# Kernel optimization log

Hardware: AMD Instinct MI355X
Metric: run time of the kernel (lower is better)

Reference implementation:

```python
import jax, jax.numpy as jnp
import numpy as np

EMBED_DIM = 1024
HIDDEN_DIM = 4096
NUM_EXPERTS = 8
TOP_K = 2


def setup_inputs() -> dict:
    key = jax.random.key(0)
    ks = jax.random.split(key, 5)
    x = jax.random.normal(ks[0], (2, 2048, EMBED_DIM), dtype=jnp.float32)
    Wg = jax.random.normal(ks[1], (EMBED_DIM, NUM_EXPERTS), dtype=jnp.float32) * 0.02
    W1 = jax.random.normal(ks[2], (NUM_EXPERTS, EMBED_DIM, HIDDEN_DIM), dtype=jnp.float32) * 0.02
    W3 = jax.random.normal(ks[3], (NUM_EXPERTS, EMBED_DIM, HIDDEN_DIM), dtype=jnp.float32) * 0.02
    W2 = jax.random.normal(ks[4], (NUM_EXPERTS, HIDDEN_DIM, EMBED_DIM), dtype=jnp.float32) * 0.02
    return {"x": x, "Wg": Wg, "W1": W1, "W3": W3, "W2": W2}


def reference(x, Wg, W1, W3, W2):
    # Gate: linear projection to num_experts logits
    gate = jnp.einsum("bsd,de->bse", x, Wg)  # [B,S,E]
    top_vals, top_idx = jax.lax.top_k(gate, TOP_K)  # [B,S,K]
    sel_w = jax.nn.softmax(top_vals, axis=-1)  # softmax over top-k values
    # Scatter selected weights into dense [B,S,E] (zeros for unselected experts)
    dense_w = jnp.sum(
        jax.nn.one_hot(top_idx, NUM_EXPERTS, dtype=sel_w.dtype) * sel_w[..., None],
        axis=-2,
    )  # [B,S,E]
    # Per-expert SwiGLU FFN; weight=0 for tokens not routed to expert e,
    # so the weighted-sum form is mathematically identical to masked dispatch.
    out = jnp.zeros_like(x)
    for e in range(NUM_EXPERTS):
        h = jax.nn.swish(jnp.einsum("bsd,dh->bsh", x, W1[e])) * jnp.einsum(
            "bsd,dh->bsh", x, W3[e]
        )
        out = out + dense_w[..., e:e + 1] * jnp.einsum("bsh,hd->bsd", h, W2[e])
    return out
```

## Files before the change

kernel.cpp:

```cpp
#include <hip/hip_runtime.h>
#include <hip/hip_bf16.h>
#include <stdint.h>

#define D_EMBED 1024
#define D_HID   4096
#define N_TOK   4096
#define N_EXP   8
#define CAP     4096
#define NROWA   8448

typedef __attribute__((ext_vector_type(4))) float f32x4;
typedef __attribute__((ext_vector_type(8))) short bf16x8;

__device__ __forceinline__ unsigned short f2bf(float f) {
    unsigned int u = __builtin_bit_cast(unsigned int, f);
    u += 0x7fffu + ((u >> 16) & 1u);
    return (unsigned short)(u >> 16);
}

__device__ __forceinline__ void gload_lds16(const void* g, void* l) {
    __builtin_amdgcn_global_load_lds(
        (const __attribute__((address_space(1))) unsigned int*)g,
        (__attribute__((address_space(3))) unsigned int*)l,
        16, 0, 0);
}

__global__ __launch_bounds__(256) void pack_w(const float* __restrict__ W,
                                              unsigned short* __restrict__ out, int R, int C) {
    int e = blockIdx.z, kb = blockIdx.y, cb = blockIdx.x;
    const float* Wp = W + (size_t)e * R * C + (size_t)(kb * 64) * C + cb * 64;
    unsigned short* op = out + (size_t)e * R * C;
    __shared__ unsigned short lds[64][72];
    int t = threadIdx.x;
    int r = t >> 2;
    int c0 = (t & 3) << 4;
    const float* src = Wp + (size_t)r * C + c0;
#pragma unroll
    for (int i = 0; i < 2; ++i) {
        f32x4 a = *reinterpret_cast<const f32x4*>(src + i * 8);
        f32x4 b = *reinterpret_cast<const f32x4*>(src + i * 8 + 4);
        bf16x8 o;
        o[0]=(short)f2bf(a[0]); o[1]=(short)f2bf(a[1]); o[2]=(short)f2bf(a[2]); o[3]=(short)f2bf(a[3]);
        o[4]=(short)f2bf(b[0]); o[5]=(short)f2bf(b[1]); o[6]=(short)f2bf(b[2]); o[7]=(short)f2bf(b[3]);
        *reinterpret_cast<bf16x8*>(&lds[r][c0 + i * 8]) = o;
    }
    __syncthreads();
#pragma unroll
    for (int i = 0; i < 2; ++i) {
        int cell = i * 256 + t;
        int ksl = cell >> 6, col = cell & 63;
        bf16x8 o;
#pragma unroll
        for (int j = 0; j < 8; ++j) o[j] = (short)lds[ksl * 8 + j][col];
        *reinterpret_cast<bf16x8*>(op + ((size_t)(kb * 8 + ksl) * C + cb * 64 + col) * 8) = o;
    }
}

__global__ __launch_bounds__(256) void pack_w13(const float* __restrict__ W1,
                                                const float* __restrict__ W3,
                                                unsigned short* __restrict__ out) {
    int e = blockIdx.z, kb = blockIdx.y, cb = blockIdx.x;
    size_t ebase = (size_t)e * D_EMBED * D_HID;
    const float* b1 = W1 + ebase + (size_t)(kb * 64) * D_HID + cb * 32;
    const float* b3 = W3 + ebase + (size_t)(kb * 64) * D_HID + cb * 32;
    unsigned short* op = out + (size_t)e * D_EMBED * 2 * D_HID;
    __shared__ unsigned short lds[64][72];
    int t = threadIdx.x;
    int r = t >> 2, ck = t & 3;
    const float* src = (ck >= 2 ? b3 : b1) + (size_t)r * D_HID + (ck & 1) * 16;
#pragma unroll
    for (int i = 0; i < 2; ++i) {
        f32x4 a = *reinterpret_cast<const f32x4*>(src + i * 8);
        f32x4 b = *reinterpret_cast<const f32x4*>(src + i * 8 + 4);
        bf16x8 o;
        o[0]=(short)f2bf(a[0]); o[1]=(short)f2bf(a[1]); o[2]=(short)f2bf(a[2]); o[3]=(short)f2bf(a[3]);
        o[4]=(short)f2bf(b[0]); o[5]=(short)f2bf(b[1]); o[6]=(short)f2bf(b[2]); o[7]=(short)f2bf(b[3]);
        *reinterpret_cast<bf16x8*>(&lds[r][ck * 16 + i * 8]) = o;
    }
    __syncthreads();
#pragma unroll
    for (int i = 0; i < 2; ++i) {
        int cell = i * 256 + t;
        int ksl = cell >> 6, pcp = cell & 63;
        int lcol = ((pcp >> 4) & 1) * 32 + ((pcp >> 5) & 1) * 16 + (pcp & 15);
        bf16x8 o;
#pragma unroll
        for (int j = 0; j < 8; ++j) o[j] = (short)lds[ksl * 8 + j][lcol];
        *reinterpret_cast<bf16x8*>(op + ((size_t)(kb * 8 + ksl) * (2 * D_HID) + cb * 64 + pcp) * 8) = o;
    }
}

__global__ __launch_bounds__(256) void gate_kernel(const float* __restrict__ x,
                                                   const float* __restrict__ Wg,
                                                   int* __restrict__ counts,
                                                   int* __restrict__ toks,
                                                   float* __restrict__ wgts,
                                                   int* __restrict__ slots) {
    int wave = threadIdx.x >> 6;
    int lane = threadIdx.x & 63;
    int tok = blockIdx.x * 4 + wave;
    const float* xp = x + (size_t)tok * D_EMBED;
    float acc[8] = {0, 0, 0, 0, 0, 0, 0, 0};
#pragma unroll
    for (int i = 0; i < 16; ++i) {
        int d = lane + 64 * i;
        float xv = xp[d];
        f32x4 w0 = *reinterpret_cast<const f32x4*>(Wg + (size_t)d * 8);
        f32x4 w1 = *reinterpret_cast<const f32x4*>(Wg + (size_t)d * 8 + 4);
        acc[0] += xv * w0[0]; acc[1] += xv * w0[1]; acc[2] += xv * w0[2]; acc[3] += xv * w0[3];
        acc[4] += xv * w1[0]; acc[5] += xv * w1[1]; acc[6] += xv * w1[2]; acc[7] += xv * w1[3];
    }
#pragma unroll
    for (int e = 0; e < 8; ++e)
        for (int s = 32; s; s >>= 1) acc[e] += __shfl_xor(acc[e], s, 64);
    if (lane == 0) {
        int i0 = 0; float v0 = acc[0];
#pragma unroll
        for (int e = 1; e < 8; ++e) if (acc[e] > v0) { v0 = acc[e]; i0 = e; }
        int i1 = -1; float v1 = -1e30f;
#pragma unroll
        for (int e = 0; e < 8; ++e) if (e != i0 && acc[e] > v1) { v1 = acc[e]; i1 = e; }
        float ex = __expf(v1 - v0);
        float w0 = 1.0f / (1.0f + ex);
        float w1 = 1.0f - w0;
        int p0 = atomicAdd(&counts[i0], 1);
        toks[i0 * CAP + p0] = tok; wgts[i0 * CAP + p0] = w0; slots[i0 * CAP + p0] = 0;
        int p1 = atomicAdd(&counts[i1], 1);
        toks[i1 * CAP + p1] = tok; wgts[i1 * CAP + p1] = w1; slots[i1 * CAP + p1] = 1;
    }
}

__global__ void prefix_kernel(const int* __restrict__ counts, int* __restrict__ offsets) {
    if (threadIdx.x == 0) {
        int s = 0;
        for (int e = 0; e < N_EXP; ++e) { offsets[e] = s; s += counts[e]; }
    }
}

__global__ __launch_bounds__(256) void build_map_kernel(const int* __restrict__ counts,
                                                        const int* __restrict__ offsets,
                                                        const int* __restrict__ toks,
                                                        const int* __restrict__ slots,
                                                        int* __restrict__ tok2row) {
    int i = blockIdx.x * 256 + threadIdx.x;
    int e = i >> 12, pos = i & (CAP - 1);
    if (pos < counts[e])
        tok2row[toks[i] * 2 + slots[i]] = offsets[e] + pos;
}

__global__ __launch_bounds__(256) void gather_x_kernel(
    const float* __restrict__ x,
    const int* __restrict__ counts, const int* __restrict__ offsets,
    const int* __restrict__ toks,
    unsigned short* __restrict__ xg) {
    int rt = blockIdx.x;
    int e = -1, base = 0, rowbase = 0, cnt = 0;
    for (int ee = 0; ee < N_EXP; ++ee) {
        int c = counts[ee];
        int nt = (c + 63) >> 6;
        if (rt < base + nt) { e = ee; rowbase = (rt - base) << 6; cnt = c; break; }
        base += nt;
    }
    if (e < 0) return;
    int off = offsets[e];
    int kb = blockIdx.y;
    __shared__ unsigned short lds[64][72];
    int t = threadIdx.x;
    int r = t >> 2, ck = t & 3;
    int pos = rowbase + r;
    unsigned short tmp[16];
    if (pos < cnt) {
        int tok = toks[e * CAP + pos];
        const float* src = x + (size_t)tok * D_EMBED + kb * 64 + ck * 16;
#pragma unroll
        for (int i = 0; i < 4; ++i) {
            f32x4 v = *reinterpret_cast<const f32x4*>(src + i * 4);
#pragma unroll
            for (int j = 0; j < 4; ++j) tmp[i * 4 + j] = f2bf(v[j]);
        }
    } else {
#pragma unroll
        for (int i = 0; i < 16; ++i) tmp[i] = 0;
    }
#pragma unroll
    for (int i = 0; i < 16; ++i) lds[r][ck * 16 + i] = tmp[i];
    __syncthreads();
    int sl = t >> 5, rr = (t & 31) * 2;
#pragma unroll
    for (int w = 0; w < 2; ++w) {
        int rw = rr + w;
        if (rowbase + rw >= cnt) continue;
        bf16x8 o;
#pragma unroll
        for (int j = 0; j < 8; ++j) o[j] = (short)lds[rw][sl * 8 + j];
        *reinterpret_cast<bf16x8*>(xg + ((size_t)(kb * 8 + sl) * NROWA + off + rowbase + rw) * 8) = o;
    }
}

__global__ __launch_bounds__(512, 1) void gemm1_kernel(
    const unsigned short* __restrict__ xg,
    const unsigned short* __restrict__ wt13,
    const int* __restrict__ counts, const int* __restrict__ offsets,
    const float* __restrict__ wgts,
    unsigned short* __restrict__ hp) {
    int rt = blockIdx.y;
    int e = -1, base = 0, rowbase = 0, cnt = 0;
#pragma unroll 1
    for (int ee = 0; ee < N_EXP; ++ee) {
        int c = counts[ee];
        int nt = (c + 255) >> 8;
        if (rt < base + nt) { e = ee; rowbase = (rt - base) << 8; cnt = c; break; }
        base += nt;
    }
    if (e < 0) return;
    int off = offsets[e];
    int colbase = blockIdx.x * 128;

    __shared__ __align__(16) char lds[3][49152];

    int t = threadIdx.x, lane = t & 63, w = t >> 6;
    int wr = w >> 1, wc = w & 1;
    int q = lane >> 4, p = lane & 15;

    const unsigned short* wB = wt13 + (size_t)e * D_EMBED * 2 * D_HID;
    const unsigned short* pA = xg + (size_t)(off + rowbase) * 8;

    f32x4 acc[4][4] = {};

    auto STAGE = [&](char* L, int kt) {
        size_t sl = (size_t)(kt * 8 + w);
#pragma unroll
        for (int qt = 0; qt < 4; ++qt)
            gload_lds16(pA + (sl * NROWA + qt * 64 + lane) * 8, L + (w * 4 + qt) * 1024);
#pragma unroll
        for (int h = 0; h < 2; ++h)
            gload_lds16(wB + (sl * (2 * D_HID) + colbase + h * 64 + lane) * 8,
                        L + 32768 + (w * 2 + h) * 1024);
    };
    auto COMPUTE = [&](const char* L) {
#pragma unroll
        for (int ks = 0; ks < 2; ++ks) {
            bf16x8 af[4], bf[4];
#pragma unroll
            for (int m = 0; m < 4; ++m)
                af[m] = *reinterpret_cast<const bf16x8*>(L + ((ks * 4 + q) * 4 + wr) * 1024 + m * 256 + p * 16);
#pragma unroll
            for (int n = 0; n < 4; ++n)
                bf[n] = *reinterpret_cast<const bf16x8*>(L + 32768 + ((ks * 4 + q) * 2 + wc) * 1024 + n * 256 + p * 16);
#pragma unroll
            for (int n = 0; n < 4; ++n)
#pragma unroll
                for (int m = 0; m < 4; ++m)
                    acc[m][n] = __builtin_amdgcn_mfma_f32_16x16x32_bf16(af[m], bf[n], acc[m][n], 0, 0, 0);
        }
    };

    char* Lc = &lds[0][0]; char* Ln = &lds[1][0]; char* Ls = &lds[2][0];
    STAGE(Lc, 0); STAGE(Ln, 1);
#pragma unroll 1
    for (int kt = 0; kt < 16; ++kt) {
        if (kt < 14) { STAGE(Ls, kt + 2); asm volatile("s_waitcnt vmcnt(12)" ::: "memory"); }
        else if (kt == 14) { asm volatile("s_waitcnt vmcnt(6)" ::: "memory"); }
        else { asm volatile("s_waitcnt vmcnt(0)" ::: "memory"); }
        __builtin_amdgcn_s_barrier();
        asm volatile("" ::: "memory");
        COMPUTE(Lc);
        asm volatile("" ::: "memory");
        __builtin_amdgcn_s_barrier();
        char* tmp = Lc; Lc = Ln; Ln = Ls; Ls = tmp;
    }

#pragma unroll
    for (int m = 0; m < 4; ++m) {
#pragma unroll
        for (int reg = 0; reg < 4; ++reg) {
            int rl = wr * 64 + m * 16 + q * 4 + reg;
            int grow = rowbase + rl;
            if (grow >= cnt) continue;
            float wgt = wgts[e * CAP + grow];
            size_t row = (size_t)(off + grow);
#pragma unroll
            for (int np = 0; np < 2; ++np) {
                float a1 = acc[m][2 * np][reg];
                float a3 = acc[m][2 * np + 1][reg];
                float hv = (a1 / (1.0f + __expf(-a1))) * a3 * wgt;
                int colg = (blockIdx.x * 4 + wc * 2 + np) * 16 + p;
                hp[((size_t)(colg >> 3) * NROWA + row) * 8 + (colg & 7)] = f2bf(hv);
            }
        }
    }
}

__global__ __launch_bounds__(512, 1) void gemm2_kernel(
    const unsigned short* __restrict__ hp,
    const unsigned short* __restrict__ wt2,
    const int* __restrict__ counts, const int* __restrict__ offsets,
    float* __restrict__ pbuf) {
    int rt = blockIdx.y;
    int e = -1, base = 0, rowbase = 0, cnt = 0;
#pragma unroll 1
    for (int ee = 0; ee < N_EXP; ++ee) {
        int c = counts[ee];
        int nt = (c + 255) >> 8;
        if (rt < base + nt) { e = ee; rowbase = (rt - base) << 8; cnt = c; break; }
        base += nt;
    }
    if (e < 0) return;
    int off = offsets[e];
    int colbase = blockIdx.x * 128;
    int s2 = blockIdx.z;

    __shared__ __align__(16) char lds[3][49152];

    int t = threadIdx.x, lane = t & 63, w = t >> 6;
    int wr = w >> 1, wc = w & 1;
    int q = lane >> 4, p = lane & 15;

    const unsigned short* wB = wt2 + (size_t)e * D_HID * D_EMBED;
    const unsigned short* pA = hp + (size_t)(off + rowbase) * 8;

    f32x4 acc[4][4] = {};

    auto STAGE = [&](char* L, int kt) {
        size_t sl = (size_t)((s2 * 32 + kt) * 8 + w);
#pragma unroll
        for (int qt = 0; qt < 4; ++qt)
            gload_lds16(pA + (sl * NROWA + qt * 64 + lane) * 8, L + (w * 4 + qt) * 1024);
#pragma unroll
        for (int h = 0; h < 2; ++h)
            gload_lds16(wB + (sl * D_EMBED + colbase + h * 64 + lane) * 8,
                        L + 32768 + (w * 2 + h) * 1024);
    };
    auto COMPUTE = [&](const char* L) {
#pragma unroll
        for (int ks = 0; ks < 2; ++ks) {
            bf16x8 af[4], bf[4];
#pragma unroll
            for (int m = 0; m < 4; ++m)
                af[m] = *reinterpret_cast<const bf16x8*>(L + ((ks * 4 + q) * 4 + wr) * 1024 + m * 256 + p * 16);
#pragma unroll
            for (int n = 0; n < 4; ++n)
                bf[n] = *reinterpret_cast<const bf16x8*>(L + 32768 + ((ks * 4 + q) * 2 + wc) * 1024 + n * 256 + p * 16);
#pragma unroll
            for (int n = 0; n < 4; ++n)
#pragma unroll
                for (int m = 0; m < 4; ++m)
                    acc[m][n] = __builtin_amdgcn_mfma_f32_16x16x32_bf16(af[m], bf[n], acc[m][n], 0, 0, 0);
        }
    };

    char* Lc = &lds[0][0]; char* Ln = &lds[1][0]; char* Ls = &lds[2][0];
    STAGE(Lc, 0); STAGE(Ln, 1);
#pragma unroll 1
    for (int kt = 0; kt < 32; ++kt) {
        if (kt < 30) { STAGE(Ls, kt + 2); asm volatile("s_waitcnt vmcnt(12)" ::: "memory"); }
        else if (kt == 30) { asm volatile("s_waitcnt vmcnt(6)" ::: "memory"); }
        else { asm volatile("s_waitcnt vmcnt(0)" ::: "memory"); }
        __builtin_amdgcn_s_barrier();
        asm volatile("" ::: "memory");
        COMPUTE(Lc);
        asm volatile("" ::: "memory");
        __builtin_amdgcn_s_barrier();
        char* tmp = Lc; Lc = Ln; Ln = Ls; Ls = tmp;
    }

    float* pb = pbuf + (size_t)s2 * 8192 * D_EMBED;
#pragma unroll
    for (int m = 0; m < 4; ++m)
#pragma unroll
        for (int reg = 0; reg < 4; ++reg) {
            int rl = wr * 64 + m * 16 + q * 4 + reg;
            int grow = rowbase + rl;
            if (grow >= cnt) continue;
            float* dst = pb + (size_t)(off + grow) * D_EMBED + colbase + wc * 64;
#pragma unroll
            for (int n = 0; n < 4; ++n) dst[n * 16 + p] = acc[m][n][reg];
        }
}

__global__ __launch_bounds__(256) void combine_kernel(const float* __restrict__ pbuf,
                                                      const int* __restrict__ tok2row,
                                                      float* __restrict__ out) {
    int i = blockIdx.x * 256 + threadIdx.x;
    int tok = i >> 8, c = (i & 255) * 4;
    int r0 = tok2row[tok * 2], r1 = tok2row[tok * 2 + 1];
    const size_t SP = (size_t)8192 * D_EMBED;
    f32x4 a0 = *reinterpret_cast<const f32x4*>(pbuf + (size_t)r0 * D_EMBED + c);
    f32x4 a1 = *reinterpret_cast<const f32x4*>(pbuf + SP + (size_t)r0 * D_EMBED + c);
    f32x4 b0 = *reinterpret_cast<const f32x4*>(pbuf + (size_t)r1 * D_EMBED + c);
    f32x4 b1 = *reinterpret_cast<const f32x4*>(pbuf + SP + (size_t)r1 * D_EMBED + c);
    *reinterpret_cast<f32x4*>(out + (size_t)tok * D_EMBED + c) = (a0 + a1) + (b0 + b1);
}

extern "C" void kernel_launch(void* const* d_in, const int* in_sizes, int n_in,
                              void* d_out, int out_size, void* d_ws, size_t ws_size,
                              hipStream_t stream) {
    const float* x  = (const float*)d_in[0];
    const float* Wg = (const float*)d_in[1];
    const float* W1 = (const float*)d_in[2];
    const float* W3 = (const float*)d_in[3];
    const float* W2 = (const float*)d_in[4];
    float* out = (float*)d_out;

    char* ws = (char*)d_ws;
    size_t szW = (size_t)N_EXP * D_EMBED * D_HID;
    unsigned short* wt13 = (unsigned short*)ws; ws += szW * 2 * 2;
    unsigned short* wt2  = (unsigned short*)ws; ws += szW * 2;
    unsigned short* hp   = (unsigned short*)ws; ws += (size_t)(D_HID / 8) * NROWA * 8 * 2;
    unsigned short* xg   = (unsigned short*)ws; ws += (size_t)(D_EMBED / 8) * NROWA * 8 * 2;
    int*   toks    = (int*)ws;   ws += (size_t)N_EXP * CAP * 4;
    float* wgts    = (float*)ws; ws += (size_t)N_EXP * CAP * 4;
    int*   slots   = (int*)ws;   ws += (size_t)N_EXP * CAP * 4;
    int*   tok2row = (int*)ws;   ws += (size_t)N_TOK * 2 * 4;
    int*   counts  = (int*)ws;   ws += 8 * 4;
    int*   offsets = (int*)ws;   ws += 8 * 4;
    float* pbuf = (float*)wt13;

    hipMemsetAsync(counts, 0, 8 * sizeof(int), stream);

    pack_w13<<<dim3(128, 16, N_EXP), 256, 0, stream>>>(W1, W3, wt13);
    pack_w<<<dim3(D_EMBED / 64, D_HID / 64, N_EXP), 256, 0, stream>>>(W2, wt2, D_HID, D_EMBED);
    gate_kernel<<<N_TOK / 4, 256, 0, stream>>>(x, Wg, counts, toks, wgts, slots);
    prefix_kernel<<<1, 64, 0, stream>>>(counts, offsets);
    build_map_kernel<<<(N_EXP * CAP) / 256, 256, 0, stream>>>(counts, offsets, toks, slots, tok2row);
    gather_x_kernel<<<dim3(136, D_EMBED / 64), 256, 0, stream>>>(x, counts, offsets, toks, xg);
    gemm1_kernel<<<dim3(64, 39), 512, 0, stream>>>(xg, wt13, counts, offsets, wgts, hp);
    gemm2_kernel<<<dim3(8, 39, 2), 512, 0, stream>>>(hp, wt2, counts, offsets, pbuf);
    combine_kernel<<<(N_TOK * 256) / 256, 256, 0, stream>>>(pbuf, tok2row, out);
}
```

Measured before the change: 564.1 us.

## Enlarge GEMM tiles to 256x256, switch to double-buffered split-phase staging, 4-way split-K

Both expert GEMMs move from 256x128 to 256x256 output tiles, with 8 waves in a 2x4 layout and 8x4 accumulators per wave, to raise arithmetic intensity and reuse of LDS data. The triple-buffered pipeline becomes a double buffer in which the A and B loads for the next k-tile are issued between two MFMA phases, and s_setprio raises priority around the MFMA bursts. GEMM2 now splits K four ways instead of two, and the combine kernel sums four partial buffers. The costs are higher register pressure, fewer blocks per GEMM, a full vmcnt(0) wait every iteration, and more partial-sum traffic in the combine step.

Result: faster. 537.4 us (-4.7%).

```diff
diff --git a/kernel.cpp b/kernel.cpp
--- a/kernel.cpp
+++ b/kernel.cpp
@@ -214,67 +214,69 @@
     }
     if (e < 0) return;
     int off = offsets[e];
-    int colbase = blockIdx.x * 128;
-
-    __shared__ __align__(16) char lds[3][49152];
+    int colp = blockIdx.x * 256;
+
+    __shared__ __align__(16) char lds[2][65536];
 
     int t = threadIdx.x, lane = t & 63, w = t >> 6;
-    int wr = w >> 1, wc = w & 1;
+    int wr = w >> 2, wc = w & 3;
     int q = lane >> 4, p = lane & 15;
 
     const unsigned short* wB = wt13 + (size_t)e * D_EMBED * 2 * D_HID;
     const unsigned short* pA = xg + (size_t)(off + rowbase) * 8;
 
-    f32x4 acc[4][4] = {};
-
-    auto STAGE = [&](char* L, int kt) {
+    f32x4 acc[8][4] = {};
+
+    auto SA = [&](char* L, int kt) {
         size_t sl = (size_t)(kt * 8 + w);
 #pragma unroll
-        for (int qt = 0; qt < 4; ++qt)
-            gload_lds16(pA + (sl * NROWA + qt * 64 + lane) * 8, L + (w * 4 + qt) * 1024);
-#pragma unroll
-        for (int h = 0; h < 2; ++h)
-            gload_lds16(wB + (sl * (2 * D_HID) + colbase + h * 64 + lane) * 8,
-                        L + 32768 + (w * 2 + h) * 1024);
-    };
-    auto COMPUTE = [&](const char* L) {
-#pragma unroll
-        for (int ks = 0; ks < 2; ++ks) {
-            bf16x8 af[4], bf[4];
-#pragma unroll
-            for (int m = 0; m < 4; ++m)
-                af[m] = *reinterpret_cast<const bf16x8*>(L + ((ks * 4 + q) * 4 + wr) * 1024 + m * 256 + p * 16);
-#pragma unroll
-            for (int n = 0; n < 4; ++n)
-                bf[n] = *reinterpret_cast<const bf16x8*>(L + 32768 + ((ks * 4 + q) * 2 + wc) * 1024 + n * 256 + p * 16);
-#pragma unroll
-            for (int n = 0; n < 4; ++n)
-#pragma unroll
-                for (int m = 0; m < 4; ++m)
-                    acc[m][n] = __builtin_amdgcn_mfma_f32_16x16x32_bf16(af[m], bf[n], acc[m][n], 0, 0, 0);
-        }
-    };
-
-    char* Lc = &lds[0][0]; char* Ln = &lds[1][0]; char* Ls = &lds[2][0];
-    STAGE(Lc, 0); STAGE(Ln, 1);
+        for (int i = 0; i < 4; ++i)
+            gload_lds16(pA + (sl * NROWA + i * 64 + lane) * 8, L + (w * 4 + i) * 1024);
+    };
+    auto SB = [&](char* L, int kt) {
+        size_t sl = (size_t)(kt * 8 + w);
+#pragma unroll
+        for (int i = 0; i < 4; ++i)
+            gload_lds16(wB + (sl * (2 * D_HID) + colp + i * 64 + lane) * 8,
+                        L + 32768 + (w * 4 + i) * 1024);
+    };
+    auto PHASE = [&](const char* L, int ks) {
+        bf16x8 af[8], bfr[4];
+#pragma unroll
+        for (int m = 0; m < 8; ++m)
+            af[m] = *reinterpret_cast<const bf16x8*>(L + (ks * 4 + q) * 4096 + (wr * 128 + m * 16 + p) * 16);
+#pragma unroll
+        for (int n = 0; n < 4; ++n)
+            bfr[n] = *reinterpret_cast<const bf16x8*>(L + 32768 + (ks * 4 + q) * 4096 + (wc * 64 + n * 16 + p) * 16);
+        __builtin_amdgcn_s_setprio(1);
+#pragma unroll
+        for (int n = 0; n < 4; ++n)
+#pragma unroll
+            for (int m = 0; m < 8; ++m)
+                acc[m][n] = __builtin_amdgcn_mfma_f32_16x16x32_bf16(af[m], bfr[n], acc[m][n], 0, 0, 0);
+        __builtin_amdgcn_s_setprio(0);
+    };
+
+    SA(&lds[0][0], 0); SB(&lds[0][0], 0);
 #pragma unroll 1
     for (int kt = 0; kt < 16; ++kt) {
-        if (kt < 14) { STAGE(Ls, kt + 2); asm volatile("s_waitcnt vmcnt(12)" ::: "memory"); }
-        else if (kt == 14) { asm volatile("s_waitcnt vmcnt(6)" ::: "memory"); }
-        else { asm volatile("s_waitcnt vmcnt(0)" ::: "memory"); }
+        asm volatile("s_waitcnt vmcnt(0)" ::: "memory");
         __builtin_amdgcn_s_barrier();
         asm volatile("" ::: "memory");
-        COMPUTE(Lc);
+        const char* Lc = &lds[kt & 1][0];
+        char* Ln = &lds[(kt & 1) ^ 1][0];
+        if (kt < 15) SA(Ln, kt + 1);
+        PHASE(Lc, 0);
+        if (kt < 15) SB(Ln, kt + 1);
+        PHASE(Lc, 1);
         asm volatile("" ::: "memory");
-        __builtin_amdgcn_s_barrier();
-        char* tmp = Lc; Lc = Ln; Ln = Ls; Ls = tmp;
-    }
-
-#pragma unroll
-    for (int m = 0; m < 4; ++m) {
+    }
+
+#pragma unroll
+    for (int m = 0; m < 8; ++m) {
 #pragma unroll
         for (int reg = 0; reg < 4; ++reg) {
-            int rl = wr * 64 + m * 16 + q * 4 + reg;
+            int rl = wr * 128 + m * 16 + q * 4 + reg;
             int grow = rowbase + rl;
             if (grow >= cnt) continue;
             float wgt = wgts[e * CAP + grow];
@@ -284,8 +286,8 @@
                 float a1 = acc[m][2 * np][reg];
                 float a3 = acc[m][2 * np + 1][reg];
                 float hv = (a1 / (1.0f + __expf(-a1))) * a3 * wgt;
-                int colg = (blockIdx.x * 4 + wc * 2 + np) * 16 + p;
-                hp[((size_t)(colg >> 3) * NROWA + row) * 8 + (colg & 7)] = f2bf(hv);
+                int rc = (blockIdx.x * 8 + wc * 2 + np) * 16 + p;
+                hp[((size_t)(rc >> 3) * NROWA + row) * 8 + (rc & 7)] = f2bf(hv);
             }
         }
     }
@@ -307,72 +309,74 @@
     }
     if (e < 0) return;
     int off = offsets[e];
-    int colbase = blockIdx.x * 128;
+    int colb = blockIdx.x * 256;
     int s2 = blockIdx.z;
 
-    __shared__ __align__(16) char lds[3][49152];
+    __shared__ __align__(16) char lds[2][65536];
 
     int t = threadIdx.x, lane = t & 63, w = t >> 6;
-    int wr = w >> 1, wc = w & 1;
+    int wr = w >> 2, wc = w & 3;
     int q = lane >> 4, p = lane & 15;
 
     const unsigned short* wB = wt2 + (size_t)e * D_HID * D_EMBED;
     const unsigned short* pA = hp + (size_t)(off + rowbase) * 8;
 
-    f32x4 acc[4][4] = {};
-
-    auto STAGE = [&](char* L, int kt) {
-        size_t sl = (size_t)((s2 * 32 + kt) * 8 + w);
-#pragma unroll
-        for (int qt = 0; qt < 4; ++qt)
-            gload_lds16(pA + (sl * NROWA + qt * 64 + lane) * 8, L + (w * 4 + qt) * 1024);
-#pragma unroll
-        for (int h = 0; h < 2; ++h)
-            gload_lds16(wB + (sl * D_EMBED + colbase + h * 64 + lane) * 8,
-                        L + 32768 + (w * 2 + h) * 1024);
-    };
-    auto COMPUTE = [&](const char* L) {
-#pragma unroll
-        for (int ks = 0; ks < 2; ++ks) {
-            bf16x8 af[4], bf[4];
-#pragma unroll
-            for (int m = 0; m < 4; ++m)
-                af[m] = *reinterpret_cast<const bf16x8*>(L + ((ks * 4 + q) * 4 + wr) * 1024 + m * 256 + p * 16);
-#pragma unroll
-            for (int n = 0; n < 4; ++n)
-                bf[n] = *reinterpret_cast<const bf16x8*>(L + 32768 + ((ks * 4 + q) * 2 + wc) * 1024 + n * 256 + p * 16);
-#pragma unroll
-            for (int n = 0; n < 4; ++n)
-#pragma unroll
-                for (int m = 0; m < 4; ++m)
-                    acc[m][n] = __builtin_amdgcn_mfma_f32_16x16x32_bf16(af[m], bf[n], acc[m][n], 0, 0, 0);
-        }
-    };
-
-    char* Lc = &lds[0][0]; char* Ln = &lds[1][0]; char* Ls = &lds[2][0];
-    STAGE(Lc, 0); STAGE(Ln, 1);
+    f32x4 acc[8][4] = {};
+
+    auto SA = [&](char* L, int kt) {
+        size_t sl = (size_t)(s2 * 128 + kt * 8 + w);
+#pragma unroll
+        for (int i = 0; i < 4; ++i)
+            gload_lds16(pA + (sl * NROWA + i * 64 + lane) * 8, L + (w * 4 + i) * 1024);
+    };
+    auto SB = [&](char* L, int kt) {
+        size_t sl = (size_t)(s2 * 128 + kt * 8 + w);
+#pragma unroll
+        for (int i = 0; i < 4; ++i)
+            gload_lds16(wB + (sl * D_EMBED + colb + i * 64 + lane) * 8,
+                        L + 32768 + (w * 4 + i) * 1024);
+    };
+    auto PHASE = [&](const char* L, int ks) {
+        bf16x8 af[8], bfr[4];
+#pragma unroll
+        for (int m = 0; m < 8; ++m)
+            af[m] = *reinterpret_cast<const bf16x8*>(L + (ks * 4 + q) * 4096 + (wr * 128 + m * 16 + p) * 16);
+#pragma unroll
+        for (int n = 0; n < 4; ++n)
+            bfr[n] = *reinterpret_cast<const bf16x8*>(L + 32768 + (ks * 4 + q) * 4096 + (wc * 64 + n * 16 + p) * 16);
+        __builtin_amdgcn_s_setprio(1);
+#pragma unroll
+        for (int n = 0; n < 4; ++n)
+#pragma unroll
+            for (int m = 0; m < 8; ++m)
+                acc[m][n] = __builtin_amdgcn_mfma_f32_16x16x32_bf16(af[m], bfr[n], acc[m][n], 0, 0, 0);
+        __builtin_amdgcn_s_setprio(0);
+    };
+
+    SA(&lds[0][0], 0); SB(&lds[0][0], 0);
 #pragma unroll 1
-    for (int kt = 0; kt < 32; ++kt) {
-        if (kt < 30) { STAGE(Ls, kt + 2); asm volatile("s_waitcnt vmcnt(12)" ::: "memory"); }
-        else if (kt == 30) { asm volatile("s_waitcnt vmcnt(6)" ::: "memory"); }
-        else { asm volatile("s_waitcnt vmcnt(0)" ::: "memory"); }
+    for (int kt = 0; kt < 16; ++kt) {
+        asm volatile("s_waitcnt vmcnt(0)" ::: "memory");
         __builtin_amdgcn_s_barrier();
         asm volatile("" ::: "memory");
-        COMPUTE(Lc);
+        const char* Lc = &lds[kt & 1][0];
+        char* Ln = &lds[(kt & 1) ^ 1][0];
+        if (kt < 15) SA(Ln, kt + 1);
+        PHASE(Lc, 0);
+        if (kt < 15) SB(Ln, kt + 1);
+        PHASE(Lc, 1);
         asm volatile("" ::: "memory");
-        __builtin_amdgcn_s_barrier();
-        char* tmp = Lc; Lc = Ln; Ln = Ls; Ls = tmp;
     }
 
     float* pb = pbuf + (size_t)s2 * 8192 * D_EMBED;
 #pragma unroll
-    for (int m = 0; m < 4; ++m)
+    for (int m = 0; m < 8; ++m)
 #pragma unroll
         for (int reg = 0; reg < 4; ++reg) {
-            int rl = wr * 64 + m * 16 + q * 4 + reg;
+            int rl = wr * 128 + m * 16 + q * 4 + reg;
             int grow = rowbase + rl;
             if (grow >= cnt) continue;
-            float* dst = pb + (size_t)(off + grow) * D_EMBED + colbase + wc * 64;
+            float* dst = pb + (size_t)(off + grow) * D_EMBED + colb + wc * 64;
 #pragma unroll
             for (int n = 0; n < 4; ++n) dst[n * 16 + p] = acc[m][n][reg];
         }
@@ -385,11 +389,14 @@
     int tok = i >> 8, c = (i & 255) * 4;
     int r0 = tok2row[tok * 2], r1 = tok2row[tok * 2 + 1];
     const size_t SP = (size_t)8192 * D_EMBED;
-    f32x4 a0 = *reinterpret_cast<const f32x4*>(pbuf + (size_t)r0 * D_EMBED + c);
-    f32x4 a1 = *reinterpret_cast<const f32x4*>(pbuf + SP + (size_t)r0 * D_EMBED + c);
-    f32x4 b0 = *reinterpret_cast<const f32x4*>(pbuf + (size_t)r1 * D_EMBED + c);
-    f32x4 b1 = *reinterpret_cast<const f32x4*>(pbuf + SP + (size_t)r1 * D_EMBED + c);
-    *reinterpret_cast<f32x4*>(out + (size_t)tok * D_EMBED + c) = (a0 + a1) + (b0 + b1);
+    f32x4 s = {0.f, 0.f, 0.f, 0.f};
+#pragma unroll
+    for (int sp = 0; sp < 4; ++sp) {
+        f32x4 a = *reinterpret_cast<const f32x4*>(pbuf + sp * SP + (size_t)r0 * D_EMBED + c);
+        f32x4 b = *reinterpret_cast<const f32x4*>(pbuf + sp * SP + (size_t)r1 * D_EMBED + c);
+        s = s + a + b;
+    }
+    *reinterpret_cast<f32x4*>(out + (size_t)tok * D_EMBED + c) = s;
 }
 
 extern "C" void kernel_launch(void* const* d_in, const int* in_sizes, int n_in,
@@ -424,7 +431,7 @@
     prefix_kernel<<<1, 64, 0, stream>>>(counts, offsets);
     build_map_kernel<<<(N_EXP * CAP) / 256, 256, 0, stream>>>(counts, offsets, toks, slots, tok2row);
     gather_x_kernel<<<dim3(136, D_EMBED / 64), 256, 0, stream>>>(x, counts, offsets, toks, xg);
-    gemm1_kernel<<<dim3(64, 39), 512, 0, stream>>>(xg, wt13, counts, offsets, wgts, hp);
-    gemm2_kernel<<<dim3(8, 39, 2), 512, 0, stream>>>(hp, wt2, counts, offsets, pbuf);
+    gemm1_kernel<<<dim3(32, 39), 512, 0, stream>>>(xg, wt13, counts, offsets, wgts, hp);
+    gemm2_kernel<<<dim3(4, 39, 4), 512, 0, stream>>>(hp, wt2, counts, offsets, pbuf);
     combine_kernel<<<(N_TOK * 256) / 256, 256, 0, stream>>>(pbuf, tok2row, out);
 }
```
